# Optimization experiments

Measured on AMD Instinct MI355X. Metric: run time of the kernel, lower is better.

## Reference

```python
import jax, jax.numpy as jnp
import numpy as np

EPS = 1e-12  # torch F.normalize eps


def setup_inputs() -> dict:
    key = jax.random.key(0)
    k1, k2, k3, k4, k5 = jax.random.split(key, 5)
    N, C, H, W = 32, 512, 32, 32
    E = 1024   # expansion * dim
    G = 8      # group
    D = E // G # 128, per-group channel dim
    K = 64     # num_clusters
    x = jax.random.normal(k1, (N, C, H, W), dtype=jnp.float32)
    W1 = jax.random.normal(k2, (E, C), dtype=jnp.float32) / np.sqrt(C)
    W2 = jax.random.normal(k3, (G, E), dtype=jnp.float32) / np.sqrt(E)
    Wc = jax.random.normal(k4, (K, D), dtype=jnp.float32) / np.sqrt(D)
    centroids = jax.random.uniform(k5, (K, D), dtype=jnp.float32)
    return {"x": x, "W1": W1, "W2": W2, "Wc": Wc, "centroids": centroids}


def reference(x, W1, W2, Wc, centroids):
    # x: [N, C, H, W]; W1: [E, C]; W2: [G, E]; Wc: [K, D]; centroids: [K, D]
    N, C, H, W = x.shape
    E = W1.shape[0]
    G = W2.shape[0]
    K, D = Wc.shape
    P = H * W
    # descriptor-wise L2 normalization over channel dim
    norm = jnp.linalg.norm(x, axis=1, keepdims=True)
    x = x / jnp.maximum(norm, EPS)
    # linear1 on channels: [N, E, P]
    xe = jnp.einsum('ncp,ec->nep', x.reshape(N, C, P), W1)
    # grouped features: [N, G, D, P]
    xg = xe.reshape(N, G, D, P)
    # attention gate: sigmoid(linear2)  -> [N, G, P]
    att = jax.nn.sigmoid(jnp.einsum('nep,ge->ngp', xe, W2))
    # 1x1 conv = per-pixel matmul with cluster weights -> [N, G, K, P]
    soft_assign = jax.nn.softmax(jnp.einsum('ngdp,kd->ngkp', xg, Wc), axis=2)
    # combined per-(cluster,pixel) weight
    w = soft_assign * att[:, :, None, :]  # [N, G, K, P]
    # NetVLAD residual aggregation, algebraically decomposed to avoid the
    # giant [N,G,K,D,P] intermediate:
    #   vlad[n,k,d] = sum_{g,p} w * xg  -  centroids[k,d] * sum_{g,p} w
    agg = jnp.einsum('ngkp,ngdp->nkd', w, xg)  # [N, K, D]
    wsum = w.sum(axis=(1, 3))                  # [N, K]
    vlad = agg - wsum[:, :, None] * centroids[None]  # [N, K, D]
    return vlad.reshape(N, K * D)
```

## Files before the change

### kernel.cpp

```cpp
#include <hip/hip_runtime.h>


#define N_  32
#define C_  512
#define P_  1024
#define E_  1024
#define G_  8
#define D_  128
#define K_  64

typedef __attribute__((ext_vector_type(8))) short bf16x8;
typedef __attribute__((ext_vector_type(4))) float f32x4;

__device__ __forceinline__ unsigned short f2b(float f) {
    union { float f; unsigned u; } v; v.f = f;
    unsigned r = (v.u + 0x7FFFu + ((v.u >> 16) & 1u)) >> 16;
    return (unsigned short)r;
}
__device__ __forceinline__ float b2f(unsigned short h) {
    union { unsigned u; float f; } v; v.u = ((unsigned)h) << 16;
    return v.f;
}

__device__ __forceinline__ void gl_lds16(const void* g, void* l) {
    __builtin_amdgcn_global_load_lds(
        (const __attribute__((address_space(1))) void*)g,
        (__attribute__((address_space(3))) void*)l, 16, 0, 0);
}

__global__ __launch_bounds__(256) void k0a_convert_w1(const float* __restrict__ W1,
                                                      unsigned short* __restrict__ W1b) {
    int i = blockIdx.x * 256 + threadIdx.x;
    W1b[i] = f2b(W1[i]);
}

__global__ __launch_bounds__(256) void k0b_make_v(const float* __restrict__ W1,
                                                  const float* __restrict__ Wc,
                                                  unsigned short* __restrict__ Vb) {
    int bid = blockIdx.x;
    int ch = bid & 1, k = (bid >> 1) & 63, g = bid >> 7;
    int c = ch * 256 + threadIdx.x;
    float acc = 0.f;
    #pragma unroll 8
    for (int d = 0; d < 128; ++d) {
        acc += Wc[k * 128 + d] * W1[(g * 128 + d) * C_ + c];
    }
    Vb[(g * 64 + k) * C_ + c] = f2b(acc);
}

__global__ __launch_bounds__(256) void k1_norm_transpose(const float* __restrict__ x,
                                                         unsigned short* __restrict__ xhat_t) {
    __shared__ float rn[64];
    __shared__ float tile[64 * 65];
    int n = blockIdx.y;
    int p0 = blockIdx.x * 64;
    int t = threadIdx.x;
    int ps = t & 63, cs = t >> 6;

    float ss = 0.f;
    for (int i = 0; i < 128; ++i) {
        int c = cs * 128 + i;
        float v = x[(n * C_ + c) * P_ + p0 + ps];
        ss += v * v;
    }
    tile[t] = ss;
    __syncthreads();
    if (t < 64) {
        float s = tile[t] + tile[64 + t] + tile[128 + t] + tile[192 + t];
        rn[t] = 1.0f / fmaxf(sqrtf(s), 1e-12f);
    }
    __syncthreads();

    for (int cb = 0; cb < C_; cb += 64) {
        #pragma unroll
        for (int i = 0; i < 16; ++i) {
            int cl = (t >> 6) * 16 + i;
            tile[cl * 65 + (t & 63)] = x[(n * C_ + cb + cl) * P_ + p0 + (t & 63)];
        }
        __syncthreads();
        #pragma unroll
        for (int pr = 0; pr < 16; ++pr) {
            int ps2 = (t >> 6) * 16 + pr;
            int cl2 = t & 63;
            float v = tile[cl2 * 65 + ps2] * rn[ps2];
            xhat_t[((size_t)(n * P_ + p0 + ps2)) * C_ + cb + cl2] = f2b(v);
        }
        __syncthreads();
    }
}

__global__ __launch_bounds__(256) void k2_gemm_xe(const unsigned short* __restrict__ W1b,
                                                  const unsigned short* __restrict__ xhat_t,
                                                  unsigned short* __restrict__ xe) {
    __shared__ __align__(16) short As[128 * 32];
    __shared__ __align__(16) short Bs[128 * 32];
    int n = blockIdx.y;
    int e0 = (blockIdx.x >> 3) * 128;
    int p0 = (blockIdx.x & 7) * 128;
    int t = threadIdx.x;
    int w = t >> 6, l = t & 63, q = l >> 4, l15 = l & 15;
    int wr = w >> 1, wc = w & 1;

    f32x4 acc[4][4];
    #pragma unroll
    for (int mi = 0; mi < 4; ++mi)
        #pragma unroll
        for (int ni = 0; ni < 4; ++ni)
            acc[mi][ni] = (f32x4){0.f, 0.f, 0.f, 0.f};

    for (int ks = 0; ks < 16; ++ks) {
        int k0 = ks * 32;
        #pragma unroll
        for (int i = 0; i < 2; ++i) {
            int ch = i * 256 + t;
            int row = ch >> 2, col = (ch & 3) * 8;
            gl_lds16(&W1b[(e0 + row) * C_ + k0 + col], &As[ch * 8]);
        }
        #pragma unroll
        for (int i = 0; i < 2; ++i) {
            int ch = i * 256 + t;
            int row = ch >> 2, col = (ch & 3) * 8;
            gl_lds16(&xhat_t[((size_t)(n * P_ + p0 + row)) * C_ + k0 + col], &Bs[ch * 8]);
        }
        __syncthreads();

        bf16x8 af[4], bf[4];
        #pragma unroll
        for (int mi = 0; mi < 4; ++mi)
            af[mi] = *(const bf16x8*)&As[(wr * 64 + mi * 16 + l15) * 32 + q * 8];
        #pragma unroll
        for (int ni = 0; ni < 4; ++ni)
            bf[ni] = *(const bf16x8*)&Bs[(wc * 64 + ni * 16 + l15) * 32 + q * 8];
        #pragma unroll
        for (int mi = 0; mi < 4; ++mi)
            #pragma unroll
            for (int ni = 0; ni < 4; ++ni)
                acc[mi][ni] = __builtin_amdgcn_mfma_f32_16x16x32_bf16(af[mi], bf[ni], acc[mi][ni], 0, 0, 0);
        __syncthreads();
    }

    #pragma unroll
    for (int mi = 0; mi < 4; ++mi) {
        #pragma unroll
        for (int ni = 0; ni < 4; ++ni) {
            #pragma unroll
            for (int r = 0; r < 4; ++r) {
                int e = e0 + wr * 64 + mi * 16 + q * 4 + r;
                int p = p0 + wc * 64 + ni * 16 + l15;
                xe[((size_t)(n * E_ + e)) * P_ + p] = f2b(acc[mi][ni][r]);
            }
        }
    }
}

__global__ __launch_bounds__(256) void k3a_att_part(const unsigned short* __restrict__ xe,
                                                    const float* __restrict__ W2,
                                                    float* __restrict__ att_part) {
    int n = blockIdx.y;
    int pblk = blockIdx.x & 3, ec = blockIdx.x >> 2;
    int p = pblk * 256 + threadIdx.x;
    int e0 = ec * 64;
    float acc[8];
    #pragma unroll
    for (int g = 0; g < 8; ++g) acc[g] = 0.f;
    #pragma unroll 8
    for (int i = 0; i < 64; ++i) {
        int e = e0 + i;
        float v = b2f(xe[((size_t)(n * E_ + e)) * P_ + p]);
        #pragma unroll
        for (int g = 0; g < 8; ++g)
            acc[g] += v * W2[g * E_ + e];
    }
    #pragma unroll
    for (int g = 0; g < 8; ++g)
        att_part[(((size_t)(n * 16 + ec)) * 8 + g) * P_ + p] = acc[g];
}

__global__ __launch_bounds__(256) void k3b_att_reduce(const float* __restrict__ att_part,
                                                      float* __restrict__ att_s) {
    int idx = blockIdx.x * 256 + threadIdx.x;
    int p = idx & 1023;
    int g = (idx >> 10) & 7;
    int n = idx >> 13;
    float s = 0.f;
    #pragma unroll
    for (int ec = 0; ec < 16; ++ec)
        s += att_part[(((size_t)(n * 16 + ec)) * 8 + g) * P_ + p];
    att_s[idx] = 1.0f / (1.0f + __expf(-s));
}

__global__ __launch_bounds__(256) void k4_assign_agg(const unsigned short* __restrict__ Vb,
                                                     const unsigned short* __restrict__ xhat_t,
                                                     const unsigned short* __restrict__ xe,
                                                     const float* __restrict__ att_s,
                                                     float* __restrict__ agg_part,
                                                     float* __restrict__ wsum_part) {
    __shared__ __align__(16) short As2[64 * 32];
    __shared__ __align__(16) short Bs2[128 * 32];
    __shared__ __align__(16) short wlds[64 * 136];
    __shared__ __align__(16) short xglds[128 * 136];

    int g = blockIdx.x & 7, ph = blockIdx.x >> 3, n = blockIdx.y;
    int t = threadIdx.x;
    int w = t >> 6, l = t & 63, q = l >> 4, l15 = l & 15;

    f32x4 acc_a[4][2];
    #pragma unroll
    for (int mi = 0; mi < 4; ++mi)
        #pragma unroll
        for (int ni = 0; ni < 2; ++ni)
            acc_a[mi][ni] = (f32x4){0.f, 0.f, 0.f, 0.f};
    float wsp[16];
    #pragma unroll
    for (int j = 0; j < 16; ++j) wsp[j] = 0.f;

    for (int cc = 0; cc < 4; ++cc) {
        int p0c = ph * 512 + cc * 128;

        f32x4 acc_s[4][2];
        #pragma unroll
        for (int mi = 0; mi < 4; ++mi)
            #pragma unroll
            for (int ni = 0; ni < 2; ++ni)
                acc_s[mi][ni] = (f32x4){0.f, 0.f, 0.f, 0.f};

        for (int ks = 0; ks < 16; ++ks) {
            int k0 = ks * 32;
            {
                int row = t >> 2, col = (t & 3) * 8;
                gl_lds16(&Vb[(g * 64 + row) * C_ + k0 + col], &As2[t * 8]);
            }
            #pragma unroll
            for (int i = 0; i < 2; ++i) {
                int ch = i * 256 + t;
                int row = ch >> 2, col = (ch & 3) * 8;
                gl_lds16(&xhat_t[((size_t)(n * P_ + p0c + row)) * C_ + k0 + col], &Bs2[ch * 8]);
            }
            __syncthreads();
            bf16x8 af[4], bf2[2];
            #pragma unroll
            for (int mi = 0; mi < 4; ++mi)
                af[mi] = *(const bf16x8*)&As2[(mi * 16 + l15) * 32 + q * 8];
            #pragma unroll
            for (int ni = 0; ni < 2; ++ni)
                bf2[ni] = *(const bf16x8*)&Bs2[(w * 32 + ni * 16 + l15) * 32 + q * 8];
            #pragma unroll
            for (int mi = 0; mi < 4; ++mi)
                #pragma unroll
                for (int ni = 0; ni < 2; ++ni)
                    acc_s[mi][ni] = __builtin_amdgcn_mfma_f32_16x16x32_bf16(af[mi], bf2[ni], acc_s[mi][ni], 0, 0, 0);
            __syncthreads();
        }

        #pragma unroll
        for (int ni = 0; ni < 2; ++ni) {
            float m = -1e30f;
            #pragma unroll
            for (int mi = 0; mi < 4; ++mi)
                #pragma unroll
                for (int r = 0; r < 4; ++r)
                    m = fmaxf(m, acc_s[mi][ni][r]);
            m = fmaxf(m, __shfl_xor(m, 16));
            m = fmaxf(m, __shfl_xor(m, 32));
            float s = 0.f;
            #pragma unroll
            for (int mi = 0; mi < 4; ++mi)
                #pragma unroll
                for (int r = 0; r < 4; ++r) {
                    float e = __expf(acc_s[mi][ni][r] - m);
                    acc_s[mi][ni][r] = e;
                    s += e;
                }
            s += __shfl_xor(s, 16);
            s += __shfl_xor(s, 32);

            int pcol = p0c + w * 32 + ni * 16 + l15;
            float av = att_s[(((size_t)(n * G_ + g)) * P_) + pcol];
            float scale = av / s;

            #pragma unroll
            for (int mi = 0; mi < 4; ++mi)
                #pragma unroll
                for (int r = 0; r < 4; ++r) {
                    float wv = acc_s[mi][ni][r] * scale;
                    wsp[mi * 4 + r] += wv;
                    wlds[(mi * 16 + q * 4 + r) * 136 + (w * 32 + ni * 16 + l15)] = (short)f2b(wv);
                }
        }

        #pragma unroll
        for (int i = 0; i < 8; ++i) {
            int ch = i * 256 + t;
            int row = ch / 17, col = (ch % 17) * 8;
            gl_lds16(&xe[((size_t)(n * E_ + g * 128 + row)) * P_ + p0c + col], &xglds[ch * 8]);
        }
        if (t < 128) {
            int ch = 2048 + t;
            int row = ch / 17, col = (ch % 17) * 8;
            gl_lds16(&xe[((size_t)(n * E_ + g * 128 + row)) * P_ + p0c + col], &xglds[ch * 8]);
        }
        __syncthreads();

        #pragma unroll
        for (int pk = 0; pk < 4; ++pk) {
            bf16x8 a2[4], b2[2];
            #pragma unroll
            for (int mi = 0; mi < 4; ++mi)
                a2[mi] = *(const bf16x8*)&wlds[(mi * 16 + l15) * 136 + pk * 32 + q * 8];
            #pragma unroll
            for (int ni = 0; ni < 2; ++ni)
                b2[ni] = *(const bf16x8*)&xglds[(w * 32 + ni * 16 + l15) * 136 + pk * 32 + q * 8];
            #pragma unroll
            for (int mi = 0; mi < 4; ++mi)
                #pragma unroll
                for (int ni = 0; ni < 2; ++ni)
                    acc_a[mi][ni] = __builtin_amdgcn_mfma_f32_16x16x32_bf16(a2[mi], b2[ni], acc_a[mi][ni], 0, 0, 0);
        }
        __syncthreads();
    }

    size_t base = (((size_t)(n * G_ + g)) * 2 + ph) * 64;
    #pragma unroll
    for (int mi = 0; mi < 4; ++mi)
        #pragma unroll
        for (int ni = 0; ni < 2; ++ni)
            #pragma unroll
            for (int r = 0; r < 4; ++r) {
                int k = mi * 16 + q * 4 + r;
                int d = w * 32 + ni * 16 + l15;
                agg_part[(base + k) * 128 + d] = acc_a[mi][ni][r];
            }

    #pragma unroll
    for (int j = 0; j < 16; ++j) {
        float v = wsp[j];
        v += __shfl_xor(v, 1);
        v += __shfl_xor(v, 2);
        v += __shfl_xor(v, 4);
        v += __shfl_xor(v, 8);
        if (l15 == 0) {
            int k = (j >> 2) * 16 + q * 4 + (j & 3);
            wsum_part[((((size_t)(n * G_ + g)) * 2 + ph) * 4 + w) * 64 + k] = v;
        }
    }
}

__global__ __launch_bounds__(256) void k5_final(const float* __restrict__ agg_part,
                                                const float* __restrict__ wsum_part,
                                                const float* __restrict__ centroids,
                                                float* __restrict__ out) {
    int idx = blockIdx.x * 256 + threadIdx.x;
    int d = idx & 127;
    int k = (idx >> 7) & 63;
    int n = idx >> 13;
    float ws = 0.f;
    #pragma unroll
    for (int g = 0; g < 8; ++g)
        #pragma unroll
        for (int ph = 0; ph < 2; ++ph)
            #pragma unroll
            for (int w2 = 0; w2 < 4; ++w2)
                ws += wsum_part[((((size_t)(n * G_ + g)) * 2 + ph) * 4 + w2) * 64 + k];
    float agg = 0.f;
    #pragma unroll
    for (int g = 0; g < 8; ++g)
        #pragma unroll
        for (int ph = 0; ph < 2; ++ph)
            agg += agg_part[(((((size_t)(n * G_ + g)) * 2 + ph) * 64) + k) * 128 + d];
    out[idx] = agg - ws * centroids[k * 128 + d];
}

extern "C" void kernel_launch(void* const* d_in, const int* in_sizes, int n_in,
                              void* d_out, int out_size, void* d_ws, size_t ws_size,
                              hipStream_t stream) {
    const float* x         = (const float*)d_in[0];
    const float* W1        = (const float*)d_in[1];
    const float* W2        = (const float*)d_in[2];
    const float* Wc        = (const float*)d_in[3];
    const float* centroids = (const float*)d_in[4];
    float* out = (float*)d_out;

    char* ws = (char*)d_ws;
    unsigned short* W1b      = (unsigned short*)(ws + 0);
    unsigned short* Vb       = (unsigned short*)(ws + 1048576);
    unsigned short* xhat_t   = (unsigned short*)(ws + 1572864);
    unsigned short* xe       = (unsigned short*)(ws + 35127296);
    float*          att_s    = (float*)(ws + 102236160);
    float*          agg_part = (float*)(ws + 103284736);
    float*          att_part = (float*)(ws + 103284736);
    float*          wsum_part= (float*)(ws + 120061952);

    hipLaunchKernelGGL(k0a_convert_w1, dim3(2048), dim3(256), 0, stream, W1, W1b);
    hipLaunchKernelGGL(k0b_make_v,     dim3(1024), dim3(256), 0, stream, W1, Wc, Vb);
    hipLaunchKernelGGL(k1_norm_transpose, dim3(16, 32), dim3(256), 0, stream, x, xhat_t);
    hipLaunchKernelGGL(k2_gemm_xe,     dim3(64, 32), dim3(256), 0, stream, W1b, xhat_t, xe);
    hipLaunchKernelGGL(k3a_att_part,   dim3(64, 32), dim3(256), 0, stream, xe, W2, att_part);
    hipLaunchKernelGGL(k3b_att_reduce, dim3(1024), dim3(256), 0, stream, att_part, att_s);
    hipLaunchKernelGGL(k4_assign_agg,  dim3(16, 32), dim3(256), 0, stream, Vb, xhat_t, xe,
                       att_s, agg_part, wsum_part);
    hipLaunchKernelGGL(k5_final,       dim3(1024), dim3(256), 0, stream,
                       agg_part, wsum_part, centroids, out);
}
```

Measured before the change: 262.7 us.

## Fuse prep kernels, single-pass norm-transpose, vectorize attention, atomic agg split

Merges the W1 conversion and V construction into one prep kernel. The norm/transpose kernel now reads x once, caching it as bf16 in LDS, and writes xhat_t with vector stores. The attention kernel switches to 4-wide vector loads per thread with fewer blocks. The aggregation kernel splits the pixel range into four quarters for more blocks, stages xe in half tiles, and accumulates into memset-zeroed buffers with float atomics, which lets the final kernel do a smaller reduction. Costs include an extra memset, atomic contention, nondeterministic summation order, and an extra bf16 rounding before normalization.

```diff
diff --git a/kernel.cpp b/kernel.cpp
--- a/kernel.cpp
+++ b/kernel.cpp
@@ -28,18 +28,17 @@
         (__attribute__((address_space(3))) void*)l, 16, 0, 0);
 }
 
-__global__ __launch_bounds__(256) void k0a_convert_w1(const float* __restrict__ W1,
-                                                      unsigned short* __restrict__ W1b) {
-    int i = blockIdx.x * 256 + threadIdx.x;
-    W1b[i] = f2b(W1[i]);
-}
-
-__global__ __launch_bounds__(256) void k0b_make_v(const float* __restrict__ W1,
-                                                  const float* __restrict__ Wc,
-                                                  unsigned short* __restrict__ Vb) {
+__global__ __launch_bounds__(256) void k0_prep(const float* __restrict__ W1,
+                                               const float* __restrict__ Wc,
+                                               unsigned short* __restrict__ W1b,
+                                               unsigned short* __restrict__ Vb) {
     int bid = blockIdx.x;
+    int t = threadIdx.x;
+    int i0 = bid * 512 + t;
+    W1b[i0]       = f2b(W1[i0]);
+    W1b[i0 + 256] = f2b(W1[i0 + 256]);
     int ch = bid & 1, k = (bid >> 1) & 63, g = bid >> 7;
-    int c = ch * 256 + threadIdx.x;
+    int c = ch * 256 + t;
     float acc = 0.f;
     #pragma unroll 8
     for (int d = 0; d < 128; ++d) {
@@ -50,8 +49,9 @@
 
 __global__ __launch_bounds__(256) void k1_norm_transpose(const float* __restrict__ x,
                                                          unsigned short* __restrict__ xhat_t) {
+    __shared__ short xc[128 * 256];
+    __shared__ float red[256];
     __shared__ float rn[64];
-    __shared__ float tile[64 * 65];
     int n = blockIdx.y;
     int p0 = blockIdx.x * 64;
     int t = threadIdx.x;
@@ -59,33 +59,27 @@
 
     float ss = 0.f;
     for (int i = 0; i < 128; ++i) {
-        int c = cs * 128 + i;
-        float v = x[(n * C_ + c) * P_ + p0 + ps];
+        float v = x[((size_t)(n * C_ + cs * 128 + i)) * P_ + p0 + ps];
         ss += v * v;
-    }
-    tile[t] = ss;
+        xc[i * 256 + t] = (short)f2b(v);
+    }
+    red[t] = ss;
     __syncthreads();
     if (t < 64) {
-        float s = tile[t] + tile[64 + t] + tile[128 + t] + tile[192 + t];
+        float s = red[t] + red[64 + t] + red[128 + t] + red[192 + t];
         rn[t] = 1.0f / fmaxf(sqrtf(s), 1e-12f);
     }
     __syncthreads();
 
-    for (int cb = 0; cb < C_; cb += 64) {
-        #pragma unroll
-        for (int i = 0; i < 16; ++i) {
-            int cl = (t >> 6) * 16 + i;
-            tile[cl * 65 + (t & 63)] = x[(n * C_ + cb + cl) * P_ + p0 + (t & 63)];
-        }
-        __syncthreads();
-        #pragma unroll
-        for (int pr = 0; pr < 16; ++pr) {
-            int ps2 = (t >> 6) * 16 + pr;
-            int cl2 = t & 63;
-            float v = tile[cl2 * 65 + ps2] * rn[ps2];
-            xhat_t[((size_t)(n * P_ + p0 + ps2)) * C_ + cb + cl2] = f2b(v);
-        }
-        __syncthreads();
+    float r = rn[ps];
+    size_t base = ((size_t)(n * P_ + p0 + ps)) * C_ + cs * 128;
+    #pragma unroll
+    for (int jj = 0; jj < 16; ++jj) {
+        bf16x8 o;
+        #pragma unroll
+        for (int j = 0; j < 8; ++j)
+            o[j] = (short)f2b(b2f((unsigned short)xc[(jj * 8 + j) * 256 + t]) * r);
+        *(bf16x8*)&xhat_t[base + jj * 8] = o;
     }
 }
 
@@ -157,23 +151,24 @@
                                                     const float* __restrict__ W2,
                                                     float* __restrict__ att_part) {
     int n = blockIdx.y;
-    int pblk = blockIdx.x & 3, ec = blockIdx.x >> 2;
-    int p = pblk * 256 + threadIdx.x;
+    int ec = blockIdx.x;
+    int t = threadIdx.x;
     int e0 = ec * 64;
-    float acc[8];
-    #pragma unroll
-    for (int g = 0; g < 8; ++g) acc[g] = 0.f;
-    #pragma unroll 8
+    f32x4 acc[8];
+    #pragma unroll
+    for (int g = 0; g < 8; ++g) acc[g] = (f32x4){0.f, 0.f, 0.f, 0.f};
+    #pragma unroll 4
     for (int i = 0; i < 64; ++i) {
         int e = e0 + i;
-        float v = b2f(xe[((size_t)(n * E_ + e)) * P_ + p]);
+        ushort4 v4 = *(const ushort4*)&xe[((size_t)(n * E_ + e)) * P_ + t * 4];
+        f32x4 vf = {b2f(v4.x), b2f(v4.y), b2f(v4.z), b2f(v4.w)};
         #pragma unroll
         for (int g = 0; g < 8; ++g)
-            acc[g] += v * W2[g * E_ + e];
+            acc[g] += vf * W2[g * E_ + e];
     }
     #pragma unroll
     for (int g = 0; g < 8; ++g)
-        att_part[(((size_t)(n * 16 + ec)) * 8 + g) * P_ + p] = acc[g];
+        *(f32x4*)&att_part[(((size_t)(n * 16 + ec)) * 8 + g) * P_ + t * 4] = acc[g];
 }
 
 __global__ __launch_bounds__(256) void k3b_att_reduce(const float* __restrict__ att_part,
@@ -193,14 +188,14 @@
                                                      const unsigned short* __restrict__ xhat_t,
                                                      const unsigned short* __restrict__ xe,
                                                      const float* __restrict__ att_s,
-                                                     float* __restrict__ agg_part,
-                                                     float* __restrict__ wsum_part) {
+                                                     float* __restrict__ agg,
+                                                     float* __restrict__ wsum) {
     __shared__ __align__(16) short As2[64 * 32];
     __shared__ __align__(16) short Bs2[128 * 32];
     __shared__ __align__(16) short wlds[64 * 136];
-    __shared__ __align__(16) short xglds[128 * 136];
-
-    int g = blockIdx.x & 7, ph = blockIdx.x >> 3, n = blockIdx.y;
+    __shared__ __align__(16) short xglds[128 * 72];
+
+    int g = blockIdx.x & 7, qh = blockIdx.x >> 3, n = blockIdx.y;
     int t = threadIdx.x;
     int w = t >> 6, l = t & 63, q = l >> 4, l15 = l & 15;
 
@@ -214,8 +209,8 @@
     #pragma unroll
     for (int j = 0; j < 16; ++j) wsp[j] = 0.f;
 
-    for (int cc = 0; cc < 4; ++cc) {
-        int p0c = ph * 512 + cc * 128;
+    for (int cc = 0; cc < 2; ++cc) {
+        int p0c = qh * 256 + cc * 128;
 
         f32x4 acc_s[4][2];
         #pragma unroll
@@ -288,38 +283,42 @@
                 }
         }
 
-        #pragma unroll
-        for (int i = 0; i < 8; ++i) {
-            int ch = i * 256 + t;
-            int row = ch / 17, col = (ch % 17) * 8;
-            gl_lds16(&xe[((size_t)(n * E_ + g * 128 + row)) * P_ + p0c + col], &xglds[ch * 8]);
-        }
-        if (t < 128) {
-            int ch = 2048 + t;
-            int row = ch / 17, col = (ch % 17) * 8;
-            gl_lds16(&xe[((size_t)(n * E_ + g * 128 + row)) * P_ + p0c + col], &xglds[ch * 8]);
-        }
-        __syncthreads();
-
-        #pragma unroll
-        for (int pk = 0; pk < 4; ++pk) {
-            bf16x8 a2[4], b2[2];
-            #pragma unroll
-            for (int mi = 0; mi < 4; ++mi)
-                a2[mi] = *(const bf16x8*)&wlds[(mi * 16 + l15) * 136 + pk * 32 + q * 8];
-            #pragma unroll
-            for (int ni = 0; ni < 2; ++ni)
-                b2[ni] = *(const bf16x8*)&xglds[(w * 32 + ni * 16 + l15) * 136 + pk * 32 + q * 8];
-            #pragma unroll
-            for (int mi = 0; mi < 4; ++mi)
+        for (int h = 0; h < 2; ++h) {
+            #pragma unroll
+            for (int i = 0; i < 4; ++i) {
+                int ch = i * 256 + t;
+                int row = ch / 9, col = (ch % 9) * 8;
+                gl_lds16(&xe[((size_t)(n * E_ + g * 128 + row)) * P_ + p0c + h * 64 + col],
+                         &xglds[ch * 8]);
+            }
+            if (t < 128) {
+                int ch = 1024 + t;
+                int row = ch / 9, col = (ch % 9) * 8;
+                gl_lds16(&xe[((size_t)(n * E_ + g * 128 + row)) * P_ + p0c + h * 64 + col],
+                         &xglds[ch * 8]);
+            }
+            __syncthreads();
+
+            #pragma unroll
+            for (int pk = 0; pk < 2; ++pk) {
+                bf16x8 a2[4], b2[2];
+                #pragma unroll
+                for (int mi = 0; mi < 4; ++mi)
+                    a2[mi] = *(const bf16x8*)&wlds[(mi * 16 + l15) * 136 + h * 64 + pk * 32 + q * 8];
                 #pragma unroll
                 for (int ni = 0; ni < 2; ++ni)
-                    acc_a[mi][ni] = __builtin_amdgcn_mfma_f32_16x16x32_bf16(a2[mi], b2[ni], acc_a[mi][ni], 0, 0, 0);
-        }
-        __syncthreads();
-    }
-
-    size_t base = (((size_t)(n * G_ + g)) * 2 + ph) * 64;
+                    b2[ni] = *(const bf16x8*)&xglds[(w * 32 + ni * 16 + l15) * 72 + pk * 32 + q * 8];
+                #pragma unroll
+                for (int mi = 0; mi < 4; ++mi)
+                    #pragma unroll
+                    for (int ni = 0; ni < 2; ++ni)
+                        acc_a[mi][ni] = __builtin_amdgcn_mfma_f32_16x16x32_bf16(a2[mi], b2[ni], acc_a[mi][ni], 0, 0, 0);
+            }
+            __syncthreads();
+        }
+    }
+
+    size_t base = ((size_t)(n * G_ + g)) * 64;
     #pragma unroll
     for (int mi = 0; mi < 4; ++mi)
         #pragma unroll
@@ -328,7 +327,7 @@
             for (int r = 0; r < 4; ++r) {
                 int k = mi * 16 + q * 4 + r;
                 int d = w * 32 + ni * 16 + l15;
-                agg_part[(base + k) * 128 + d] = acc_a[mi][ni][r];
+                atomicAdd(&agg[(base + k) * 128 + d], acc_a[mi][ni][r]);
             }
 
     #pragma unroll
@@ -340,34 +339,27 @@
         v += __shfl_xor(v, 8);
         if (l15 == 0) {
             int k = (j >> 2) * 16 + q * 4 + (j & 3);
-            wsum_part[((((size_t)(n * G_ + g)) * 2 + ph) * 4 + w) * 64 + k] = v;
-        }
-    }
-}
-
-__global__ __launch_bounds__(256) void k5_final(const float* __restrict__ agg_part,
-                                                const float* __restrict__ wsum_part,
+            atomicAdd(&wsum[base + k], v);
+        }
+    }
+}
+
+__global__ __launch_bounds__(256) void k5_final(const float* __restrict__ agg,
+                                                const float* __restrict__ wsum,
                                                 const float* __restrict__ centroids,
                                                 float* __restrict__ out) {
     int idx = blockIdx.x * 256 + threadIdx.x;
     int d = idx & 127;
     int k = (idx >> 7) & 63;
     int n = idx >> 13;
-    float ws = 0.f;
-    #pragma unroll
-    for (int g = 0; g < 8; ++g)
-        #pragma unroll
-        for (int ph = 0; ph < 2; ++ph)
-            #pragma unroll
-            for (int w2 = 0; w2 < 4; ++w2)
-                ws += wsum_part[((((size_t)(n * G_ + g)) * 2 + ph) * 4 + w2) * 64 + k];
-    float agg = 0.f;
-    #pragma unroll
-    for (int g = 0; g < 8; ++g)
-        #pragma unroll
-        for (int ph = 0; ph < 2; ++ph)
-            agg += agg_part[(((((size_t)(n * G_ + g)) * 2 + ph) * 64) + k) * 128 + d];
-    out[idx] = agg - ws * centroids[k * 128 + d];
+    float ws = 0.f, ag = 0.f;
+    #pragma unroll
+    for (int g = 0; g < 8; ++g) {
+        size_t base = ((size_t)(n * G_ + g)) * 64 + k;
+        ws += wsum[base];
+        ag += agg[base * 128 + d];
+    }
+    out[idx] = ag - ws * centroids[k * 128 + d];
 }
 
 extern "C" void kernel_launch(void* const* d_in, const int* in_sizes, int n_in,
@@ -381,23 +373,23 @@
     float* out = (float*)d_out;
 
     char* ws = (char*)d_ws;
-    unsigned short* W1b      = (unsigned short*)(ws + 0);
-    unsigned short* Vb       = (unsigned short*)(ws + 1048576);
-    unsigned short* xhat_t   = (unsigned short*)(ws + 1572864);
-    unsigned short* xe       = (unsigned short*)(ws + 35127296);
-    float*          att_s    = (float*)(ws + 102236160);
-    float*          agg_part = (float*)(ws + 103284736);
+    unsigned short* W1b    = (unsigned short*)(ws + 0);
+    unsigned short* Vb     = (unsigned short*)(ws + 1048576);
+    unsigned short* xhat_t = (unsigned short*)(ws + 1572864);
+    unsigned short* xe     = (unsigned short*)(ws + 35127296);
+    float*          att_s  = (float*)(ws + 102236160);
     float*          att_part = (float*)(ws + 103284736);
-    float*          wsum_part= (float*)(ws + 120061952);
-
-    hipLaunchKernelGGL(k0a_convert_w1, dim3(2048), dim3(256), 0, stream, W1, W1b);
-    hipLaunchKernelGGL(k0b_make_v,     dim3(1024), dim3(256), 0, stream, W1, Wc, Vb);
+    float*          agg    = (float*)(ws + 103284736);
+    float*          wsum   = (float*)(ws + 111673344);
+
+    hipLaunchKernelGGL(k0_prep,        dim3(1024), dim3(256), 0, stream, W1, Wc, W1b, Vb);
     hipLaunchKernelGGL(k1_norm_transpose, dim3(16, 32), dim3(256), 0, stream, x, xhat_t);
     hipLaunchKernelGGL(k2_gemm_xe,     dim3(64, 32), dim3(256), 0, stream, W1b, xhat_t, xe);
-    hipLaunchKernelGGL(k3a_att_part,   dim3(64, 32), dim3(256), 0, stream, xe, W2, att_part);
+    hipLaunchKernelGGL(k3a_att_part,   dim3(16, 32), dim3(256), 0, stream, xe, W2, att_part);
     hipLaunchKernelGGL(k3b_att_reduce, dim3(1024), dim3(256), 0, stream, att_part, att_s);
-    hipLaunchKernelGGL(k4_assign_agg,  dim3(16, 32), dim3(256), 0, stream, Vb, xhat_t, xe,
-                       att_s, agg_part, wsum_part);
+    hipMemsetAsync(ws + 103284736, 0, 8388608 + 65536, stream);
+    hipLaunchKernelGGL(k4_assign_agg,  dim3(32, 32), dim3(256), 0, stream, Vb, xhat_t, xe,
+                       att_s, agg, wsum);
     hipLaunchKernelGGL(k5_final,       dim3(1024), dim3(256), 0, stream,
-                       agg_part, wsum_part, centroids, out);
-}
+                       agg, wsum, centroids, out);
+}
```

New measurement: 279.5 us. +6.4%, slower.
